# Kernel optimization log

Measured on AMD Instinct MI355X. Metric: run time of the kernel, lower is better.

## Reference

```python
import jax, jax.numpy as jnp
import numpy as np

REST = 0.0
DECAY = 0.5
THRESHOLD = 0.5
SG_WIDTH = 1.0  # rectangular surrogate-gradient window width

@jax.custom_vjp
def spike(v):
    return (v > THRESHOLD).astype(v.dtype)

def _spike_fwd(v):
    return spike(v), v

def _spike_bwd(v, g):
    # rectangular surrogate: d spike / d v = 1/width * 1[|v - threshold| < width/2]
    grad = (jnp.abs(v - THRESHOLD) < (SG_WIDTH * 0.5)).astype(g.dtype) / SG_WIDTH
    return (g * grad,)

spike.defvjp(_spike_fwd, _spike_bwd)

def setup_inputs() -> dict:
    key = jax.random.key(0)
    k1, k2, k3 = jax.random.split(key, 3)
    T, B, N = 128, 128, 1024
    tx = jax.random.normal(k1, (T, B, N), dtype=jnp.float32)
    lim = 1.0 / np.sqrt(N)  # nn.Linear default init range
    W = jax.random.uniform(k2, (N, N), dtype=jnp.float32, minval=-lim, maxval=lim)
    b = jax.random.uniform(k3, (N,), dtype=jnp.float32, minval=-lim, maxval=lim)
    return {"tx": tx, "W": W, "b": b}

def reference(tx, W, b):
    # tx: [T, B, N]; W: [N, N] (nn.Linear weight, applied as y @ W.T + b)
    v0 = jnp.full_like(tx[0], REST)
    y0 = jnp.zeros_like(tx[0])

    def step(carry, x):
        v, y = carry
        x = x + y @ W.T + b                      # recurrent input
        v = DECAY * v * (1.0 - y) + REST * y + x  # leaky integrate with reset
        y = spike(v)                              # threshold fire
        return (v, y), y

    _, ty = jax.lax.scan(step, (v0, y0), tx)
    return ty  # [T, B, N]
```

## Files before the change

### kernel.cpp

```cpp
#include <hip/hip_runtime.h>
#include <stdint.h>

#define TT 128
#define BB 128
#define NN 1024


typedef unsigned short ushort8 __attribute__((ext_vector_type(8)));

__device__ __forceinline__ float bfbits2f(uint32_t lo16) {
  union { uint32_t i; float f; } c;
  c.i = lo16 << 16;
  return c.f;
}

__global__ __launch_bounds__(256) void w_transpose_repack(
    float* __restrict__ W, uint16_t* __restrict__ WtBf,
    uint32_t* __restrict__ dirty) {
  __shared__ float ta[32][33];
  __shared__ float tb[32][33];

  int rem = blockIdx.x;
  int I = 0;
  while (rem >= (32 - I)) { rem -= (32 - I); ++I; }
  const int J = I + rem;

  const int lx = threadIdx.x & 31;
  const int ly = threadIdx.x >> 5;
  uint32_t bad = 0;

  if (I == J) {
#pragma unroll
    for (int i = 0; i < 4; ++i)
      ta[ly + i * 8][lx] = W[(I * 32 + ly + i * 8) * NN + J * 32 + lx];
    __syncthreads();
#pragma unroll
    for (int i = 0; i < 4; ++i) {
      const int idx = (I * 32 + ly + i * 8) * NN + J * 32 + lx;
      const float v = ta[lx][ly + i * 8];
      const uint32_t bits = __float_as_uint(v);
      W[idx] = v;
      WtBf[idx] = (uint16_t)(bits >> 16);
      bad |= (bits & 0xFFFFu);
    }
  } else {
#pragma unroll
    for (int i = 0; i < 4; ++i) {
      ta[ly + i * 8][lx] = W[(I * 32 + ly + i * 8) * NN + J * 32 + lx];
      tb[ly + i * 8][lx] = W[(J * 32 + ly + i * 8) * NN + I * 32 + lx];
    }
    __syncthreads();
#pragma unroll
    for (int i = 0; i < 4; ++i) {
      const int idxA = (J * 32 + ly + i * 8) * NN + I * 32 + lx;
      const float va = ta[lx][ly + i * 8];
      const uint32_t bitsA = __float_as_uint(va);
      W[idxA] = va;
      WtBf[idxA] = (uint16_t)(bitsA >> 16);
      bad |= (bitsA & 0xFFFFu);

      const int idxB = (I * 32 + ly + i * 8) * NN + J * 32 + lx;
      const float vb = tb[lx][ly + i * 8];
      const uint32_t bitsB = __float_as_uint(vb);
      W[idxB] = vb;
      WtBf[idxB] = (uint16_t)(bitsB >> 16);
      bad |= (bitsB & 0xFFFFu);
    }
  }
  const unsigned long long bm = __ballot(bad != 0);
  if ((threadIdx.x & 63) == 0 && bm) atomicOr(dirty, 1u);
}

__global__ __launch_bounds__(512) void lif_half(
    const void* __restrict__ tx_raw, const float* __restrict__ bias,
    const float* __restrict__ WtF32, const uint16_t* __restrict__ WtBf,
    const uint32_t* __restrict__ dirty,
    unsigned long long* __restrict__ gmask, float* __restrict__ out) {
  const int bb = blockIdx.x;
  const int b = bb & 127;
  const int h = bb >> 7;
  const int pp = bb ^ 128;
  const int tid = threadIdx.x;
  const int lane = tid & 63;
  const int wv = tid >> 6;
  const int n = (h << 9) + tid;

  __shared__ uint16_t lst[NN] __attribute__((aligned(16)));
  __shared__ unsigned long long smask[16];
  __shared__ int sprobe;

  if (tid == 0) sprobe = 0;
  __syncthreads();
  {
    const uint32_t* txw = (const uint32_t*)tx_raw;
    int local = 0;
#pragma unroll
    for (int i = 0; i < 2; ++i) {
      const uint32_t f = (txw[tid * 2 + i] >> 7) & 0xFFu;
      local += (f >= 0x74u && f < 0x81u) ? 1 : 0;
    }
    atomicAdd(&sprobe, local);
  }
  __syncthreads();
  const bool tx_is_bf16 = (sprobe > 512);
  const bool w_bf = (*dirty == 0u);

  const uint16_t* __restrict__ txh = (const uint16_t*)tx_raw;
  const float* __restrict__ txf = (const float*)tx_raw;
  const float bz = bias[n];

  const uint16_t* __restrict__ rowB = WtBf + n;
  const float* __restrict__ rowF = WtF32 + n;

  float v = 0.0f;
  int y = 0;

  auto gB = [&](int pbase, int cnt) -> float {
    float acc = 0.0f;
    for (int i = 0; i < cnt; i += 32) {
      const ushort8* lp = (const ushort8*)(lst + pbase + i);
      const ushort8 a0 = lp[0];
      const ushort8 a1 = lp[1];
      const ushort8 a2 = lp[2];
      const ushort8 a3 = lp[3];
      float wbuf[32];
#pragma unroll
      for (int u = 0; u < 8; ++u) {
        const int k = __builtin_amdgcn_readfirstlane((int)a0[u]);
        wbuf[u] = bfbits2f((uint32_t)rowB[k << 10]);
      }
#pragma unroll
      for (int u = 0; u < 8; ++u) {
        const int k = __builtin_amdgcn_readfirstlane((int)a1[u]);
        wbuf[8 + u] = bfbits2f((uint32_t)rowB[k << 10]);
      }
#pragma unroll
      for (int u = 0; u < 8; ++u) {
        const int k = __builtin_amdgcn_readfirstlane((int)a2[u]);
        wbuf[16 + u] = bfbits2f((uint32_t)rowB[k << 10]);
      }
#pragma unroll
      for (int u = 0; u < 8; ++u) {
        const int k = __builtin_amdgcn_readfirstlane((int)a3[u]);
        wbuf[24 + u] = bfbits2f((uint32_t)rowB[k << 10]);
      }
#pragma unroll
      for (int u = 0; u < 32; ++u) acc += wbuf[u];
    }
    return acc;
  };

  auto gF = [&](int s, int e) -> float {
    float acc = 0.0f;
    int i = s;
    for (; i + 8 <= e; i += 8) {
      float w[8];
#pragma unroll
      for (int u = 0; u < 8; ++u) {
        const int k = __builtin_amdgcn_readfirstlane((int)lst[i + u]);
        w[u] = rowF[k << 10];
      }
#pragma unroll
      for (int u = 0; u < 8; ++u) acc += w[u];
    }
    for (; i < e; ++i) {
      const int k = __builtin_amdgcn_readfirstlane((int)lst[i]);
      acc += rowF[k << 10];
    }
    return acc;
  };

  for (int t = 0; t < TT; ++t) {
    const int sl = t & 3;
    const unsigned long long m = __ballot(y);
    if (lane == 0) smask[h * 8 + wv] = m;
    if (lane < 2) {
      const uint32_t word = (lane == 0) ? (uint32_t)m : (uint32_t)(m >> 32);
      const unsigned long long cell =
          ((unsigned long long)(t + 1) << 32) | (unsigned long long)word;
      __hip_atomic_store(&gmask[((size_t)bb * 4 + sl) * 16 + wv * 2 + lane],
                         cell, __ATOMIC_RELAXED, __HIP_MEMORY_SCOPE_AGENT);
    }

    const int off = (t * BB + b) * NN + n;
    float xx;
    if (tx_is_bf16)
      xx = bfbits2f((uint32_t)__builtin_nontemporal_load(&txh[off]));
    else
      xx = __builtin_nontemporal_load(&txf[off]);

    __syncthreads();
    if (tid < 16) {
      const size_t ci = ((size_t)pp * 4 + sl) * 16 + tid;
      unsigned long long cell;
      while (((cell = __hip_atomic_load(&gmask[ci], __ATOMIC_RELAXED,
                                        __HIP_MEMORY_SCOPE_AGENT)) >>
              32) != (unsigned long long)(t + 1)) {
        __builtin_amdgcn_s_sleep(1);
      }
      ((uint32_t*)smask)[(1 - h) * 16 + tid] = (uint32_t)cell;
    }
    __syncthreads();

    unsigned long long mk[16];
    int cnt[16];
#pragma unroll
    for (int i = 0; i < 16; ++i) {
      mk[i] = smask[i];
      cnt[i] = __popcll(mk[i]);
    }
    int pref[16];
    {
      int s = 0;
#pragma unroll
      for (int j = 0; j < 6; ++j) { pref[j] = s; s += cnt[j]; }
    }
    {
      int s = 384;
#pragma unroll
      for (int j = 6; j < 12; ++j) { pref[j] = s; s += cnt[j]; }
    }
    {
      int s = 768;
#pragma unroll
      for (int j = 12; j < 16; ++j) { pref[j] = s; s += cnt[j]; }
    }
    const int c0 = pref[5] + cnt[5];
    const int c1 = pref[11] + cnt[11] - 384;
    const int c2 = pref[15] + cnt[15] - 768;

#pragma unroll
    for (int jj = 0; jj < 2; ++jj) {
      const int j = wv * 2 + jj;
      const unsigned long long bits = mk[j];
      if ((bits >> lane) & 1ull) {
        const int below = __builtin_amdgcn_mbcnt_hi(
            (uint32_t)(bits >> 32),
            __builtin_amdgcn_mbcnt_lo((uint32_t)bits, 0));
        lst[pref[j] + below] = (uint16_t)(j * 64 + lane);
      }
    }
    if (tid < 96) {
      const int p = tid >> 5, jn = tid & 31;
      const int c = (p == 0) ? c0 : ((p == 1) ? c1 : c2);
      if (c + jn < ((c + 31) & ~31)) lst[p * 384 + c + jn] = (uint16_t)NN;
    }
    __syncthreads();

    float P0, P1, P2;
    if (w_bf) {
      P0 = gB(0, (c0 + 31) & ~31);
      P1 = gB(384, (c1 + 31) & ~31);
      P2 = gB(768, (c2 + 31) & ~31);
    } else {
      P0 = gF(0, c0);
      P1 = gF(384, 384 + c1);
      P2 = gF(768, 768 + c2);
    }
    const float a = (P0 + P1) + P2;

    const float xv = (xx + a) + bz;
    v = (y ? 0.0f : 0.5f * v) + xv;
    y = (v > 0.5f);

    __builtin_nontemporal_store(y ? 1.0f : 0.0f, &out[off]);
  }
}

__global__ __launch_bounds__(1024) void lif_persample(
    const void* __restrict__ tx_raw, const float* __restrict__ bias,
    const float* __restrict__ WtF32, const uint16_t* __restrict__ WtBf,
    const uint32_t* __restrict__ dirty, float* __restrict__ out) {
  const int b = blockIdx.x;
  const int tid = threadIdx.x;
  const int lane = tid & 63;
  const int wv = tid >> 6;

  __shared__ uint16_t lst[NN] __attribute__((aligned(16)));
  __shared__ int wcnt[16];
  __shared__ int sprobe;

  if (tid == 0) sprobe = 0;
  __syncthreads();
  {
    const uint32_t* txw = (const uint32_t*)tx_raw;
    int local = 0;
#pragma unroll
    for (int i = 0; i < 2; ++i) {
      const uint32_t f = (txw[tid * 2 + i] >> 7) & 0xFFu;
      local += (f >= 0x74u && f < 0x81u) ? 1 : 0;
    }
    atomicAdd(&sprobe, local);
  }
  __syncthreads();
  const bool tx_is_bf16 = (sprobe > 1024);
  const bool w_bf = (*dirty == 0u);

  const uint16_t* __restrict__ txh = (const uint16_t*)tx_raw;
  const float* __restrict__ txf = (const float*)tx_raw;
  const float bz = bias[tid];

  const int pidx = (wv < 6) ? 0 : ((wv < 12) ? 1 : 2);
  const int pw0 = (pidx == 0) ? 0 : ((pidx == 1) ? 6 : 12);

  const uint16_t* __restrict__ rowB = WtBf + tid;
  const float* __restrict__ rowF = WtF32 + tid;

  float v = 0.0f;
  int y = 0;

  auto gB = [&](int pbase, int cnt) -> float {
    float acc = 0.0f;
    for (int i = 0; i < cnt; i += 32) {
      const ushort8* lp = (const ushort8*)(lst + pbase + i);
      const ushort8 a0 = lp[0];
      const ushort8 a1 = lp[1];
      const ushort8 a2 = lp[2];
      const ushort8 a3 = lp[3];
      float wbuf[32];
#pragma unroll
      for (int u = 0; u < 8; ++u) {
        const int k = __builtin_amdgcn_readfirstlane((int)a0[u]);
        wbuf[u] = bfbits2f((uint32_t)rowB[k << 10]);
      }
#pragma unroll
      for (int u = 0; u < 8; ++u) {
        const int k = __builtin_amdgcn_readfirstlane((int)a1[u]);
        wbuf[8 + u] = bfbits2f((uint32_t)rowB[k << 10]);
      }
#pragma unroll
      for (int u = 0; u < 8; ++u) {
        const int k = __builtin_amdgcn_readfirstlane((int)a2[u]);
        wbuf[16 + u] = bfbits2f((uint32_t)rowB[k << 10]);
      }
#pragma unroll
      for (int u = 0; u < 8; ++u) {
        const int k = __builtin_amdgcn_readfirstlane((int)a3[u]);
        wbuf[24 + u] = bfbits2f((uint32_t)rowB[k << 10]);
      }
#pragma unroll
      for (int u = 0; u < 32; ++u) acc += wbuf[u];
    }
    return acc;
  };

  auto gF = [&](int s, int e) -> float {
    float acc = 0.0f;
    int i = s;
    for (; i + 8 <= e; i += 8) {
      float w[8];
#pragma unroll
      for (int u = 0; u < 8; ++u) {
        const int k = __builtin_amdgcn_readfirstlane((int)lst[i + u]);
        w[u] = rowF[k << 10];
      }
#pragma unroll
      for (int u = 0; u < 8; ++u) acc += w[u];
    }
    for (; i < e; ++i) {
      const int k = __builtin_amdgcn_readfirstlane((int)lst[i]);
      acc += rowF[k << 10];
    }
    return acc;
  };

  for (int t = 0; t < TT; ++t) {
    const unsigned long long m = __ballot(y);
    if (lane == 0) wcnt[wv] = __popcll(m);
    __syncthreads();
    int base = 0, c0 = 0, c1 = 0, c2 = 0;
#pragma unroll
    for (int w = 0; w < 16; ++w) {
      const int c = wcnt[w];
      c0 += (w < 6) ? c : 0;
      c1 += (w >= 6 && w < 12) ? c : 0;
      c2 += (w >= 12) ? c : 0;
      base += (w >= pw0 && w < wv) ? c : 0;
    }
    if (y) {
      const int below = __builtin_amdgcn_mbcnt_hi(
          (uint32_t)(m >> 32), __builtin_amdgcn_mbcnt_lo((uint32_t)m, 0));
      lst[pidx * 384 + base + below] = (uint16_t)tid;
    }
    if (tid < 96) {
      const int p = tid >> 5, jn = tid & 31;
      const int c = (p == 0) ? c0 : ((p == 1) ? c1 : c2);
      if (c + jn < ((c + 31) & ~31)) lst[p * 384 + c + jn] = (uint16_t)NN;
    }
    __syncthreads();

    float P0, P1, P2;
    if (w_bf) {
      P0 = gB(0, (c0 + 31) & ~31);
      P1 = gB(384, (c1 + 31) & ~31);
      P2 = gB(768, (c2 + 31) & ~31);
    } else {
      P0 = gF(0, c0);
      P1 = gF(384, 384 + c1);
      P2 = gF(768, 768 + c2);
    }
    const float a = (P0 + P1) + P2;

    const int off = (t * BB + b) * NN + tid;
    const float xx = tx_is_bf16
        ? bfbits2f((uint32_t)__builtin_nontemporal_load(&txh[off]))
        : __builtin_nontemporal_load(&txf[off]);
    const float xv = (xx + a) + bz;
    v = (y ? 0.0f : 0.5f * v) + xv;
    y = (v > 0.5f);

    __builtin_nontemporal_store(y ? 1.0f : 0.0f, &out[off]);
  }
}

extern "C" void kernel_launch(void* const* d_in, const int* in_sizes, int n_in,
                              void* d_out, int out_size, void* d_ws, size_t ws_size,
                              hipStream_t stream) {
  const void* tx = nullptr;
  float* W = nullptr;
  const float* bs = nullptr;
  for (int i = 0; i < n_in; ++i) {
    if (in_sizes[i] == TT * BB * NN) tx = d_in[i];
    else if (in_sizes[i] == NN * NN) W = (float*)d_in[i];
    else if (in_sizes[i] == NN) bs = (const float*)d_in[i];
  }
  float* out = (float*)d_out;

  const size_t MB2 = 2u * 1024u * 1024u;
  uint16_t* WtBf = (uint16_t*)d_ws;
  uint16_t* zrow = WtBf + NN * NN;
  uint32_t* dirty = (uint32_t*)((char*)d_ws + MB2 + 2048u);
  unsigned long long* gmask =
      (unsigned long long*)((char*)d_ws + MB2 + 4096u);
  const size_t GMASK_BYTES = 256u * 4u * 16u * 8u;
  const size_t need = MB2 + 4096u + GMASK_BYTES;

  hipMemsetAsync(dirty, 0, sizeof(uint32_t), stream);
  hipMemsetAsync(zrow, 0, NN * sizeof(uint16_t), stream);

  w_transpose_repack<<<dim3(528), dim3(256), 0, stream>>>(W, WtBf, dirty);

  if (ws_size >= need) {
    hipMemsetAsync(gmask, 0, GMASK_BYTES, stream);
    lif_half<<<dim3(256), dim3(512), 0, stream>>>(tx, bs, W, WtBf, dirty,
                                                  gmask, out);
  } else {
    lif_persample<<<dim3(BB), dim3(1024), 0, stream>>>(tx, bs, W, WtBf, dirty,
                                                       out);
  }
}
```

Before: 1.720 ms.

## Stage active bf16 weight rows into LDS via async global_load_lds triple buffering

Replaces the per-thread scalar gather of bf16 weight rows with cooperative direct-to-LDS loads. Each wave loads two whole 1KB half-rows per chunk of 16 active spike indices into a three-deep shared buffer, overlapping with the accumulation of earlier chunks. Threads then sum their column from LDS, which removes the many narrow 2-byte global loads. The cost is extra LDS usage (about 48KB), two barriers per chunk, and hand-written waitcnt sequencing that depends on the ordering of outstanding loads.

```diff
diff --git a/kernel.cpp b/kernel.cpp
--- a/kernel.cpp
+++ b/kernel.cpp
@@ -12,6 +12,12 @@
   union { uint32_t i; float f; } c;
   c.i = lo16 << 16;
   return c.f;
+}
+
+__device__ __forceinline__ void gload_lds16(const void* g, void* l) {
+  __builtin_amdgcn_global_load_lds(
+      (const __attribute__((address_space(1))) uint32_t*)g,
+      (__attribute__((address_space(3))) uint32_t*)l, 16, 0, 0);
 }
 
 __global__ __launch_bounds__(256) void w_transpose_repack(
@@ -85,6 +91,7 @@
   const int wv = tid >> 6;
   const int n = (h << 9) + tid;
 
+  __shared__ uint16_t sbuf[3][16][512] __attribute__((aligned(16)));
   __shared__ uint16_t lst[NN] __attribute__((aligned(16)));
   __shared__ unsigned long long smask[16];
   __shared__ int sprobe;
@@ -109,46 +116,13 @@
   const float* __restrict__ txf = (const float*)tx_raw;
   const float bz = bias[n];
 
-  const uint16_t* __restrict__ rowB = WtBf + n;
+  const char* __restrict__ wbase = (const char*)WtBf;
   const float* __restrict__ rowF = WtF32 + n;
+  const size_t lane16 = (size_t)(lane << 4);
+  const size_t hoff = (size_t)(h << 10);
 
   float v = 0.0f;
   int y = 0;
-
-  auto gB = [&](int pbase, int cnt) -> float {
-    float acc = 0.0f;
-    for (int i = 0; i < cnt; i += 32) {
-      const ushort8* lp = (const ushort8*)(lst + pbase + i);
-      const ushort8 a0 = lp[0];
-      const ushort8 a1 = lp[1];
-      const ushort8 a2 = lp[2];
-      const ushort8 a3 = lp[3];
-      float wbuf[32];
-#pragma unroll
-      for (int u = 0; u < 8; ++u) {
-        const int k = __builtin_amdgcn_readfirstlane((int)a0[u]);
-        wbuf[u] = bfbits2f((uint32_t)rowB[k << 10]);
-      }
-#pragma unroll
-      for (int u = 0; u < 8; ++u) {
-        const int k = __builtin_amdgcn_readfirstlane((int)a1[u]);
-        wbuf[8 + u] = bfbits2f((uint32_t)rowB[k << 10]);
-      }
-#pragma unroll
-      for (int u = 0; u < 8; ++u) {
-        const int k = __builtin_amdgcn_readfirstlane((int)a2[u]);
-        wbuf[16 + u] = bfbits2f((uint32_t)rowB[k << 10]);
-      }
-#pragma unroll
-      for (int u = 0; u < 8; ++u) {
-        const int k = __builtin_amdgcn_readfirstlane((int)a3[u]);
-        wbuf[24 + u] = bfbits2f((uint32_t)rowB[k << 10]);
-      }
-#pragma unroll
-      for (int u = 0; u < 32; ++u) acc += wbuf[u];
-    }
-    return acc;
-  };
 
   auto gF = [&](int s, int e) -> float {
     float acc = 0.0f;
@@ -240,18 +214,71 @@
         lst[pref[j] + below] = (uint16_t)(j * 64 + lane);
       }
     }
-    if (tid < 96) {
-      const int p = tid >> 5, jn = tid & 31;
+    if (tid < 48) {
+      const int p = tid >> 4, jn = tid & 15;
       const int c = (p == 0) ? c0 : ((p == 1) ? c1 : c2);
-      if (c + jn < ((c + 31) & ~31)) lst[p * 384 + c + jn] = (uint16_t)NN;
-    }
-    __syncthreads();
-
-    float P0, P1, P2;
+      if (c + jn < ((c + 15) & ~15)) lst[p * 384 + c + jn] = (uint16_t)NN;
+    }
+    __syncthreads();
+
+    float P0 = 0.0f, P1 = 0.0f, P2 = 0.0f;
     if (w_bf) {
-      P0 = gB(0, (c0 + 31) & ~31);
-      P1 = gB(384, (c1 + 31) & ~31);
-      P2 = gB(768, (c2 + 31) & ~31);
+      const int n0c = (c0 + 15) >> 4;
+      const int n1c = (c1 + 15) >> 4;
+      const int n2c = (c2 + 15) >> 4;
+      const int nct = n0c + n1c + n2c;
+
+      int ka = 0, kb = 0;
+      auto readk = [&](int c) {
+        int pb;
+        if (c < n0c) pb = c * 16;
+        else if (c < n0c + n1c) pb = 384 + (c - n0c) * 16;
+        else pb = 768 + (c - n0c - n1c) * 16;
+        ka = (int)lst[pb + wv * 2];
+        kb = (int)lst[pb + wv * 2 + 1];
+      };
+      auto stage2 = [&](int cb) {
+        gload_lds16(wbase + ((size_t)ka << 11) + hoff + lane16,
+                    &sbuf[cb][wv * 2 + 0][0]);
+        gload_lds16(wbase + ((size_t)kb << 11) + hoff + lane16,
+                    &sbuf[cb][wv * 2 + 1][0]);
+      };
+
+      if (nct > 0) {
+        readk(0); stage2(0);
+        if (nct > 1) { readk(1); stage2(1); }
+        if (nct > 2) readk(2);
+        for (int c = 0; c < nct; ++c) {
+          const int cb = c - (c / 3) * 3;
+          if (c + 2 < nct) {
+            const int tb = (c + 2) - ((c + 2) / 3) * 3;
+            stage2(tb);
+            if (c + 3 < nct) readk(c + 3);
+          }
+          if (c + 2 < nct)
+            asm volatile("s_waitcnt vmcnt(4)\n\ts_barrier" ::: "memory");
+          else if (c + 1 < nct)
+            asm volatile("s_waitcnt vmcnt(2)\n\ts_barrier" ::: "memory");
+          else
+            asm volatile("s_waitcnt vmcnt(0)\n\ts_barrier" ::: "memory");
+
+          const uint16_t* rp = &sbuf[cb][0][tid];
+          if (c < n0c) {
+#pragma unroll
+            for (int r = 0; r < 16; ++r)
+              P0 += bfbits2f((uint32_t)rp[r * 512]);
+          } else if (c < n0c + n1c) {
+#pragma unroll
+            for (int r = 0; r < 16; ++r)
+              P1 += bfbits2f((uint32_t)rp[r * 512]);
+          } else {
+#pragma unroll
+            for (int r = 0; r < 16; ++r)
+              P2 += bfbits2f((uint32_t)rp[r * 512]);
+          }
+          asm volatile("s_barrier" ::: "memory");
+        }
+      }
     } else {
       P0 = gF(0, c0);
       P1 = gF(384, 384 + c1);
```

After: 1.741 ms. About the same (+1.2%).

## Stage spiking weight rows into LDS via async global_load_lds double buffering

Applied to the files above, without the earlier changes.

Each thread now handles two neurons, and the block size drops from 512 to 256. The bf16 weight gather no longer issues a scalar-indexed 2-byte load per active row. Instead, whole 1 KB half-rows are copied into a double-buffered LDS tile with global_load_lds and summed from LDS, giving wide coalesced transfers that overlap with compute. The ballot masks are bit-interleaved so the spike-mask layout stays the same for the peer block. The cost is 64 KB of shared memory per block, extra barriers per 32-row chunk, and half as many threads to hide latency.

```diff
diff --git a/kernel.cpp b/kernel.cpp
--- a/kernel.cpp
+++ b/kernel.cpp
@@ -12,6 +12,18 @@
   union { uint32_t i; float f; } c;
   c.i = lo16 << 16;
   return c.f;
+}
+
+__device__ __forceinline__ float bits2f(uint32_t b) {
+  union { uint32_t i; float f; } c;
+  c.i = b;
+  return c.f;
+}
+
+__device__ __forceinline__ void gload_lds16(const void* g, void* l) {
+  __builtin_amdgcn_global_load_lds(
+      (const __attribute__((address_space(1))) uint32_t*)g,
+      (__attribute__((address_space(3))) uint32_t*)l, 16, 0, 0);
 }
 
 __global__ __launch_bounds__(256) void w_transpose_repack(
@@ -71,7 +83,7 @@
   if ((threadIdx.x & 63) == 0 && bm) atomicOr(dirty, 1u);
 }
 
-__global__ __launch_bounds__(512) void lif_half(
+__global__ __launch_bounds__(256) void lif_half(
     const void* __restrict__ tx_raw, const float* __restrict__ bias,
     const float* __restrict__ WtF32, const uint16_t* __restrict__ WtBf,
     const uint32_t* __restrict__ dirty,
@@ -83,8 +95,9 @@
   const int tid = threadIdx.x;
   const int lane = tid & 63;
   const int wv = tid >> 6;
-  const int n = (h << 9) + tid;
-
+  const int n0 = (h << 9) + tid * 2;
+
+  __shared__ uint16_t sbuf[2][32][512] __attribute__((aligned(16)));
   __shared__ uint16_t lst[NN] __attribute__((aligned(16)));
   __shared__ unsigned long long smask[16];
   __shared__ int sprobe;
@@ -95,8 +108,8 @@
     const uint32_t* txw = (const uint32_t*)tx_raw;
     int local = 0;
 #pragma unroll
-    for (int i = 0; i < 2; ++i) {
-      const uint32_t f = (txw[tid * 2 + i] >> 7) & 0xFFu;
+    for (int i = 0; i < 4; ++i) {
+      const uint32_t f = (txw[tid * 4 + i] >> 7) & 0xFFu;
       local += (f >= 0x74u && f < 0x81u) ? 1 : 0;
     }
     atomicAdd(&sprobe, local);
@@ -107,87 +120,59 @@
 
   const uint16_t* __restrict__ txh = (const uint16_t*)tx_raw;
   const float* __restrict__ txf = (const float*)tx_raw;
-  const float bz = bias[n];
-
-  const uint16_t* __restrict__ rowB = WtBf + n;
-  const float* __restrict__ rowF = WtF32 + n;
-
-  float v = 0.0f;
-  int y = 0;
-
-  auto gB = [&](int pbase, int cnt) -> float {
-    float acc = 0.0f;
-    for (int i = 0; i < cnt; i += 32) {
-      const ushort8* lp = (const ushort8*)(lst + pbase + i);
-      const ushort8 a0 = lp[0];
-      const ushort8 a1 = lp[1];
-      const ushort8 a2 = lp[2];
-      const ushort8 a3 = lp[3];
-      float wbuf[32];
-#pragma unroll
-      for (int u = 0; u < 8; ++u) {
-        const int k = __builtin_amdgcn_readfirstlane((int)a0[u]);
-        wbuf[u] = bfbits2f((uint32_t)rowB[k << 10]);
-      }
-#pragma unroll
-      for (int u = 0; u < 8; ++u) {
-        const int k = __builtin_amdgcn_readfirstlane((int)a1[u]);
-        wbuf[8 + u] = bfbits2f((uint32_t)rowB[k << 10]);
-      }
-#pragma unroll
-      for (int u = 0; u < 8; ++u) {
-        const int k = __builtin_amdgcn_readfirstlane((int)a2[u]);
-        wbuf[16 + u] = bfbits2f((uint32_t)rowB[k << 10]);
-      }
-#pragma unroll
-      for (int u = 0; u < 8; ++u) {
-        const int k = __builtin_amdgcn_readfirstlane((int)a3[u]);
-        wbuf[24 + u] = bfbits2f((uint32_t)rowB[k << 10]);
-      }
-#pragma unroll
-      for (int u = 0; u < 32; ++u) acc += wbuf[u];
-    }
-    return acc;
-  };
-
-  auto gF = [&](int s, int e) -> float {
-    float acc = 0.0f;
-    int i = s;
-    for (; i + 8 <= e; i += 8) {
-      float w[8];
-#pragma unroll
-      for (int u = 0; u < 8; ++u) {
-        const int k = __builtin_amdgcn_readfirstlane((int)lst[i + u]);
-        w[u] = rowF[k << 10];
-      }
-#pragma unroll
-      for (int u = 0; u < 8; ++u) acc += w[u];
-    }
-    for (; i < e; ++i) {
-      const int k = __builtin_amdgcn_readfirstlane((int)lst[i]);
-      acc += rowF[k << 10];
-    }
-    return acc;
+  const float2 bz2 = *(const float2*)(bias + n0);
+
+  const char* __restrict__ wbase = (const char*)WtBf;
+  const size_t lane16 = (size_t)(lane << 4);
+  const size_t hoff = (size_t)(h << 10);
+
+  float v0 = 0.0f, v1 = 0.0f;
+  int y0 = 0, y1 = 0;
+
+  auto spread = [](uint32_t x) -> unsigned long long {
+    unsigned long long z = x;
+    z = (z | (z << 16)) & 0x0000FFFF0000FFFFull;
+    z = (z | (z << 8))  & 0x00FF00FF00FF00FFull;
+    z = (z | (z << 4))  & 0x0F0F0F0F0F0F0F0Full;
+    z = (z | (z << 2))  & 0x3333333333333333ull;
+    z = (z | (z << 1))  & 0x5555555555555555ull;
+    return z;
   };
 
   for (int t = 0; t < TT; ++t) {
     const int sl = t & 3;
-    const unsigned long long m = __ballot(y);
-    if (lane == 0) smask[h * 8 + wv] = m;
-    if (lane < 2) {
-      const uint32_t word = (lane == 0) ? (uint32_t)m : (uint32_t)(m >> 32);
+    const unsigned long long b0 = __ballot(y0);
+    const unsigned long long b1 = __ballot(y1);
+    const unsigned long long m0 =
+        spread((uint32_t)b0) | (spread((uint32_t)b1) << 1);
+    const unsigned long long m1 =
+        spread((uint32_t)(b0 >> 32)) | (spread((uint32_t)(b1 >> 32)) << 1);
+    if (lane == 0) {
+      smask[h * 8 + 2 * wv] = m0;
+      smask[h * 8 + 2 * wv + 1] = m1;
+    }
+    if (lane < 4) {
+      const unsigned long long msel = (lane & 2) ? m1 : m0;
+      const uint32_t word = (lane & 1) ? (uint32_t)(msel >> 32) : (uint32_t)msel;
       const unsigned long long cell =
           ((unsigned long long)(t + 1) << 32) | (unsigned long long)word;
-      __hip_atomic_store(&gmask[((size_t)bb * 4 + sl) * 16 + wv * 2 + lane],
+      __hip_atomic_store(&gmask[((size_t)bb * 4 + sl) * 16 + wv * 4 + lane],
                          cell, __ATOMIC_RELAXED, __HIP_MEMORY_SCOPE_AGENT);
     }
 
-    const int off = (t * BB + b) * NN + n;
-    float xx;
-    if (tx_is_bf16)
-      xx = bfbits2f((uint32_t)__builtin_nontemporal_load(&txh[off]));
-    else
-      xx = __builtin_nontemporal_load(&txf[off]);
+    const int off = (t * BB + b) * NN + n0;
+    float x0, x1;
+    if (tx_is_bf16) {
+      const uint32_t w =
+          __builtin_nontemporal_load((const uint32_t*)&txh[off]);
+      x0 = bits2f(w << 16);
+      x1 = bits2f(w & 0xFFFF0000u);
+    } else {
+      const uint64_t w2 =
+          __builtin_nontemporal_load((const uint64_t*)&txf[off]);
+      x0 = bits2f((uint32_t)w2);
+      x1 = bits2f((uint32_t)(w2 >> 32));
+    }
 
     __syncthreads();
     if (tid < 16) {
@@ -230,8 +215,8 @@
     const int c2 = pref[15] + cnt[15] - 768;
 
 #pragma unroll
-    for (int jj = 0; jj < 2; ++jj) {
-      const int j = wv * 2 + jj;
+    for (int jj = 0; jj < 4; ++jj) {
+      const int j = wv * 4 + jj;
       const unsigned long long bits = mk[j];
       if ((bits >> lane) & 1ull) {
         const int below = __builtin_amdgcn_mbcnt_hi(
@@ -247,23 +232,82 @@
     }
     __syncthreads();
 
-    float P0, P1, P2;
+    float P0a = 0.0f, P0b = 0.0f, P1a = 0.0f, P1b = 0.0f,
+          P2a = 0.0f, P2b = 0.0f;
     if (w_bf) {
-      P0 = gB(0, (c0 + 31) & ~31);
-      P1 = gB(384, (c1 + 31) & ~31);
-      P2 = gB(768, (c2 + 31) & ~31);
+      const int n0c = (c0 + 31) >> 5;
+      const int n1c = (c1 + 31) >> 5;
+      const int n2c = (c2 + 31) >> 5;
+      const int nct = n0c + n1c + n2c;
+
+      auto stage = [&](int c, int cb) {
+        int rb;
+        if (c < n0c) rb = c * 32;
+        else if (c < n0c + n1c) rb = 384 + (c - n0c) * 32;
+        else rb = 768 + (c - n0c - n1c) * 32;
+        const ushort8 kv = *(const ushort8*)(lst + rb + wv * 8);
+#pragma unroll
+        for (int j = 0; j < 8; ++j) {
+          const int k = __builtin_amdgcn_readfirstlane((int)kv[j]);
+          gload_lds16(wbase + ((size_t)k << 11) + hoff + lane16,
+                      &sbuf[cb][wv * 8 + j][0]);
+        }
+      };
+      auto consume32 = [&](int cb, float& A, float& B) {
+        const uint32_t* rp = (const uint32_t*)(&sbuf[cb][0][0]) + tid;
+#pragma unroll
+        for (int r = 0; r < 32; ++r) {
+          const uint32_t w = rp[r * 256];
+          A += bits2f(w << 16);
+          B += bits2f(w & 0xFFFF0000u);
+        }
+      };
+
+      if (nct > 0) {
+        stage(0, 0);
+        if (nct > 1) stage(1, 1);
+        for (int c = 0; c < nct; ++c) {
+          const int cb = c & 1;
+          if (c + 1 < nct)
+            asm volatile("s_waitcnt vmcnt(8)\n\ts_barrier" ::: "memory");
+          else
+            asm volatile("s_waitcnt vmcnt(0)\n\ts_barrier" ::: "memory");
+
+          if (c < n0c) consume32(cb, P0a, P0b);
+          else if (c < n0c + n1c) consume32(cb, P1a, P1b);
+          else consume32(cb, P2a, P2b);
+
+          asm volatile("s_barrier" ::: "memory");
+          if (c + 2 < nct) stage(c + 2, cb);
+        }
+      }
     } else {
-      P0 = gF(0, c0);
-      P1 = gF(384, 384 + c1);
-      P2 = gF(768, 768 + c2);
-    }
-    const float a = (P0 + P1) + P2;
-
-    const float xv = (xx + a) + bz;
-    v = (y ? 0.0f : 0.5f * v) + xv;
-    y = (v > 0.5f);
-
-    __builtin_nontemporal_store(y ? 1.0f : 0.0f, &out[off]);
+      auto gF2 = [&](int s, int e, float& A, float& B) {
+        for (int i = s; i < e; ++i) {
+          const int k = __builtin_amdgcn_readfirstlane((int)lst[i]);
+          const float2 w = *(const float2*)(WtF32 + ((size_t)k << 10) + n0);
+          A += w.x;
+          B += w.y;
+        }
+      };
+      gF2(0, c0, P0a, P0b);
+      gF2(384, 384 + c1, P1a, P1b);
+      gF2(768, 768 + c2, P2a, P2b);
+    }
+    const float a0 = (P0a + P1a) + P2a;
+    const float a1 = (P0b + P1b) + P2b;
+
+    const float xv0 = (x0 + a0) + bz2.x;
+    const float xv1 = (x1 + a1) + bz2.y;
+    v0 = (y0 ? 0.0f : 0.5f * v0) + xv0;
+    v1 = (y1 ? 0.0f : 0.5f * v1) + xv1;
+    y0 = (v0 > 0.5f);
+    y1 = (v1 > 0.5f);
+
+    const uint32_t f0 = y0 ? 0x3F800000u : 0u;
+    const uint32_t f1 = y1 ? 0x3F800000u : 0u;
+    __builtin_nontemporal_store(((uint64_t)f1 << 32) | (uint64_t)f0,
+                                (uint64_t*)&out[off]);
   }
 }
 
@@ -442,7 +486,7 @@
 
   if (ws_size >= need) {
     hipMemsetAsync(gmask, 0, GMASK_BYTES, stream);
-    lif_half<<<dim3(256), dim3(512), 0, stream>>>(tx, bs, W, WtBf, dirty,
+    lif_half<<<dim3(256), dim3(256), 0, stream>>>(tx, bs, W, WtBf, dirty,
                                                   gmask, out);
   } else {
     lif_persample<<<dim3(BB), dim3(1024), 0, stream>>>(tx, bs, W, WtBf, dirty,
```

Result: slower. 5.127 ms (+198.0%).
